# Kernel optimization log

Measured on AMD Instinct MI355X. Metric: run time of the kernel, lower is better.

The kernel has to match this reference:

```python
import jax, jax.numpy as jnp
import numpy as np

B, S, H = 32, 256, 256
D = 2 * H          # BiLSTM output dim (hidden_dim*2)
F = 1024           # total fragment count across the batch
T = 5              # tagset size


def setup_inputs() -> dict:
    key = jax.random.key(0)
    ks = jax.random.split(key, 9)
    en_output = jax.random.normal(ks[0], (B, S, D), jnp.float32)
    # descending lengths, first sentence defines seq_length = S
    lengths = jnp.sort(jax.random.randint(ks[1], (B,), S // 2, S + 1))[::-1]
    lengths = lengths.at[0].set(S)
    frag_b = jax.random.randint(ks[2], (F,), 0, B)
    frag_s = jax.random.randint(ks[3], (F,), 0, S // 2 - 8)
    width = jax.random.randint(ks[4], (F,), 1, 8)
    frag_e = frag_s + width  # end exclusive, always <= lengths[frag_b]
    att_w = jax.random.normal(ks[5], (3 * D, D), jnp.float32) / np.float32(np.sqrt(3 * D))
    att_b = jax.random.normal(ks[6], (3 * D,), jnp.float32) * 0.01
    tag_w = jax.random.normal(ks[7], (T, 4 * D), jnp.float32) / np.float32(np.sqrt(4 * D))
    tag_b = jax.random.normal(ks[8], (T,), jnp.float32) * 0.01
    return {"en_output": en_output, "lengths": lengths, "frag_b": frag_b,
            "frag_s": frag_s, "frag_e": frag_e, "att_w": att_w, "att_b": att_b,
            "tag_w": tag_w, "tag_b": tag_b}


def reference(en_output, lengths, frag_b, frag_s, frag_e, att_w, att_b, tag_w, tag_b):
    Fn = frag_b.shape[0]
    Bn, Sn, Dn = en_output.shape
    dtype = en_output.dtype
    pos = jnp.arange(Sn)                                            # [S]
    in_span = (pos[None, :] >= frag_s[:, None]) & (pos[None, :] < frag_e[:, None])  # [F,S]
    memory = en_output[frag_b]                                      # [F,S,D] gather per fragment
    # word_state = sum of hidden states over the span (segment-sum via mask)
    word_state = jnp.einsum('fs,fsd->fd', in_span.astype(dtype), memory)
    l_word = en_output[frag_b, frag_s]                              # [F,D]
    r_word = en_output[frag_b, frag_e - 1]                          # [F,D]
    span = jnp.concatenate([l_word, word_state, r_word], axis=-1)   # [F,3D]
    # attention mask: the span itself and all padding positions are masked out
    att_mask = in_span | (pos[None, :] >= lengths[frag_b][:, None])  # [F,S]
    seq_len = lengths[0]
    # position distance (int), then position weight 1 - dist/seq_len
    pos_dis = jnp.where(pos[None, :] < frag_s[:, None], frag_s[:, None] - pos[None, :],
                jnp.where(pos[None, :] >= frag_e[:, None], pos[None, :] - frag_e[:, None] + 1,
                          seq_len)).astype(dtype)
    pos_weight = 1.0 - pos_dis / seq_len.astype(dtype)
    final = pos_weight[:, :, None] * memory                         # [F,S,D]
    # att(final) @ span == final @ (att_w.T span) + att_b.span ; att_w is [3D, D] (torch Linear weight)
    v = span @ att_w                                                # [F,D]
    c = span @ att_b                                                # [F]
    scores = jnp.tanh(jnp.einsum('fsd,fd->fs', final, v) + c[:, None])
    scores = jnp.where(att_mask, jnp.asarray(-1e4, dtype), scores)
    att = jax.nn.softmax(scores, axis=1)                            # [F,S]
    mix = jnp.einsum('fs,fsd->fd', att, final)                      # [F,D]
    mix_state = jnp.concatenate([span, mix], axis=-1)               # [F,4D]
    logits = mix_state @ tag_w.T + tag_b                            # [F,T]
    return jax.nn.log_softmax(logits, axis=1)
```

## Files before the change

### kernel.cpp

```cpp
#include <hip/hip_runtime.h>
#include <math.h>

#define BB 32
#define SS 256
#define DD 512
#define FF 1024
#define TT 5
#define K3 1536
#define K4 2048
#define GK 1536
#define SK 4
#define KCH (GK / SK)

__device__ __forceinline__ float wave_reduce_sum(float x) {
#pragma unroll
  for (int o = 32; o > 0; o >>= 1) x += __shfl_xor(x, o);
  return x;
}

__device__ __forceinline__ float fast_tanh(float x) {
  float ax = fabsf(x);
  float t = __expf(-2.f * ax);
  float r = (1.f - t) / (1.f + t);
  return x < 0.f ? -r : r;
}

__global__ __launch_bounds__(1024)
void bucket_kernel(const int* __restrict__ fb, int* __restrict__ order) {
  __shared__ int cnt[BB];
  __shared__ int start[BB];
  int t = threadIdx.x;
  if (t < BB) cnt[t] = 0;
  __syncthreads();
  int b = fb[t];
  int r = atomicAdd(&cnt[b], 1);
  __syncthreads();
  if (t == 0) {
    int acc = 0;
    for (int i = 0; i < BB; ++i) { start[i] = acc; acc += cnt[i]; }
  }
  __syncthreads();
  order[start[b] + r] = t;
}

__global__ __launch_bounds__(128)
void span_kernel(const float* __restrict__ en, const int* __restrict__ fb,
                 const int* __restrict__ fs, const int* __restrict__ fe,
                 const float* __restrict__ att_b,
                 float* __restrict__ span, float* __restrict__ cvec)
{
  int f = blockIdx.x;
  int t = threadIdx.x;
  int b = fb[f], s = fs[f], e = fe[f];
  const float* base = en + (size_t)b * SS * DD;
  int d0 = t * 4;
  float4 lw = *(const float4*)(base + (size_t)s * DD + d0);
  float4 rw = *(const float4*)(base + (size_t)(e - 1) * DD + d0);
  float4 wsum = make_float4(0.f, 0.f, 0.f, 0.f);
  for (int p = s; p < e; ++p) {
    float4 m = *(const float4*)(base + (size_t)p * DD + d0);
    wsum.x += m.x; wsum.y += m.y; wsum.z += m.z; wsum.w += m.w;
  }
  float* sp = span + (size_t)f * K3;
  *(float4*)(sp + d0) = lw;
  *(float4*)(sp + DD + d0) = wsum;
  *(float4*)(sp + 2 * DD + d0) = rw;
  float4 a0 = *(const float4*)(att_b + d0);
  float4 a1 = *(const float4*)(att_b + DD + d0);
  float4 a2 = *(const float4*)(att_b + 2 * DD + d0);
  float part = lw.x*a0.x + lw.y*a0.y + lw.z*a0.z + lw.w*a0.w
             + wsum.x*a1.x + wsum.y*a1.y + wsum.z*a1.z + wsum.w*a1.w
             + rw.x*a2.x + rw.y*a2.y + rw.z*a2.z + rw.w*a2.w;
  part = wave_reduce_sum(part);
  __shared__ float red[2];
  if ((t & 63) == 0) red[t >> 6] = part;
  __syncthreads();
  if (t == 0) cvec[f] = red[0] + red[1];
}

__global__ __launch_bounds__(256)
void gemm_v(const float* __restrict__ A,
            const float* __restrict__ Bw,
            float* __restrict__ Cpart)
{
  const int BM = 32, BN = 64, BK = 16;
  __shared__ float As[BK][BM + 2];
  __shared__ float Bs[BK][BN + 4];
  int t = threadIdx.x;
  int n0 = blockIdx.x * BN;
  int m0 = blockIdx.y * BM;
  int sk = blockIdx.z;
  int kbase = sk * KCH;

  int ar = t >> 3;
  int ac = (t & 7) * 2;
  int br = t >> 4;
  int bc = (t & 15) * 4;
  int tm = (t >> 4) * 2;
  int tn = (t & 15) * 4;

  float acc[2][4] = {};

  for (int k0 = kbase; k0 < kbase + KCH; k0 += BK) {
    float2 av = *(const float2*)(A + (size_t)(m0 + ar) * GK + k0 + ac);
    float4 bv = *(const float4*)(Bw + (size_t)(k0 + br) * DD + n0 + bc);
    __syncthreads();
    As[ac][ar] = av.x;
    As[ac + 1][ar] = av.y;
    *(float4*)(&Bs[br][bc]) = bv;
    __syncthreads();
#pragma unroll
    for (int k = 0; k < BK; ++k) {
      float a0 = As[k][tm], a1 = As[k][tm + 1];
      float4 b = *(float4*)(&Bs[k][tn]);
      acc[0][0] += a0 * b.x; acc[0][1] += a0 * b.y; acc[0][2] += a0 * b.z; acc[0][3] += a0 * b.w;
      acc[1][0] += a1 * b.x; acc[1][1] += a1 * b.y; acc[1][2] += a1 * b.z; acc[1][3] += a1 * b.w;
    }
  }
  float* Cp = Cpart + (size_t)sk * FF * DD;
#pragma unroll
  for (int i = 0; i < 2; ++i) {
    *(float4*)(Cp + (size_t)(m0 + tm + i) * DD + n0 + tn) =
        make_float4(acc[i][0], acc[i][1], acc[i][2], acc[i][3]);
  }
}

__global__ __launch_bounds__(256)
void frag_kernel(const float* __restrict__ en, const int* __restrict__ lengths,
                 const int* __restrict__ fb, const int* __restrict__ fs,
                 const int* __restrict__ fe,
                 const float* __restrict__ span, const float* __restrict__ cvec,
                 const float* __restrict__ vpart,
                 const float* __restrict__ tag_w, const float* __restrict__ tag_b,
                 const int* __restrict__ order,
                 float* __restrict__ out)
{
  __shared__ float v_lds[DD];
  __shared__ float buf[4][DD];
  __shared__ float mstate[4][2];
  __shared__ float mix_lds[DD];
  __shared__ float pl[4 * TT];
  __shared__ float l5[TT];

  int bid = blockIdx.x;
  int f = order[(bid & 7) * (FF / 8) + (bid >> 3)];
  int t = threadIdx.x;
  int lane = t & 63, wv = t >> 6;
  int b = fb[f], s = fs[f], e = fe[f];
  int lenb = lengths[b];
  float seqlen = (float)lengths[0];
  float c = cvec[f];
  const float* mem = en + (size_t)b * SS * DD;

  if (t < 128) {
    float4 v0 = *(const float4*)(vpart + (size_t)f * DD + t * 4);
    float4 v1 = *(const float4*)(vpart + (size_t)FF * DD + (size_t)f * DD + t * 4);
    float4 v2 = *(const float4*)(vpart + 2 * (size_t)FF * DD + (size_t)f * DD + t * 4);
    float4 v3 = *(const float4*)(vpart + 3 * (size_t)FF * DD + (size_t)f * DD + t * 4);
    *(float4*)(v_lds + t * 4) = make_float4(v0.x + v1.x + v2.x + v3.x,
                                            v0.y + v1.y + v2.y + v3.y,
                                            v0.z + v1.z + v2.z + v3.z,
                                            v0.w + v1.w + v2.w + v3.w);
  }
  __syncthreads();

  float4 va = *(float4*)(v_lds + lane * 8);
  float4 vb = *(float4*)(v_lds + lane * 8 + 4);
  float m = -1e30f, ssum = 0.f;
  float am[8] = {0.f, 0.f, 0.f, 0.f, 0.f, 0.f, 0.f, 0.f};

  for (int i0 = 0; i0 < 64; i0 += 8) {
    float4 R0[8], R1[8];
    float d8[8];
#pragma unroll
    for (int k = 0; k < 8; ++k) {
      int p = wv * 64 + i0 + k;
      const float* row = mem + (size_t)p * DD + lane * 8;
      R0[k] = *(const float4*)(row);
      R1[k] = *(const float4*)(row + 4);
      d8[k] = R0[k].x*va.x + R0[k].y*va.y + R0[k].z*va.z + R0[k].w*va.w
            + R1[k].x*vb.x + R1[k].y*vb.y + R1[k].z*vb.z + R1[k].w*vb.w;
    }
#pragma unroll
    for (int o = 32; o > 0; o >>= 1) {
#pragma unroll
      for (int k = 0; k < 8; ++k) d8[k] += __shfl_xor(d8[k], o);
    }
#pragma unroll
    for (int k = 0; k < 8; ++k) {
      int p = wv * 64 + i0 + k;
      bool mask = (p >= s && p < e) || (p >= lenb);
      if (!mask) {
        float dis = (p < s) ? (float)(s - p) : (float)(p - e + 1);
        float pw = 1.f - dis / seqlen;
        float sc = fast_tanh(pw * d8[k] + c);
        if (sc > m) {
          float scale = __expf(m - sc);
          ssum *= scale;
#pragma unroll
          for (int j = 0; j < 8; ++j) am[j] *= scale;
          m = sc;
        }
        float u = __expf(sc - m);
        ssum += u;
        float upw = u * pw;
        am[0] += upw * R0[k].x; am[1] += upw * R0[k].y; am[2] += upw * R0[k].z; am[3] += upw * R0[k].w;
        am[4] += upw * R1[k].x; am[5] += upw * R1[k].y; am[6] += upw * R1[k].z; am[7] += upw * R1[k].w;
      }
    }
  }
  if (lane == 0) { mstate[wv][0] = m; mstate[wv][1] = ssum; }
  __syncthreads();
  float M = fmaxf(fmaxf(mstate[0][0], mstate[1][0]), fmaxf(mstate[2][0], mstate[3][0]));
  float S = mstate[0][1] * __expf(mstate[0][0] - M)
          + mstate[1][1] * __expf(mstate[1][0] - M)
          + mstate[2][1] * __expf(mstate[2][0] - M)
          + mstate[3][1] * __expf(mstate[3][0] - M);
  float ew = __expf(m - M);
  {
    float4 s0 = make_float4(am[0] * ew, am[1] * ew, am[2] * ew, am[3] * ew);
    float4 s1 = make_float4(am[4] * ew, am[5] * ew, am[6] * ew, am[7] * ew);
    *(float4*)(&buf[wv][lane * 8]) = s0;
    *(float4*)(&buf[wv][lane * 8 + 4]) = s1;
  }
  __syncthreads();
  {
    int d0 = t * 2;
    float inv = 1.f / S;
    mix_lds[d0]     = (buf[0][d0] + buf[1][d0] + buf[2][d0] + buf[3][d0]) * inv;
    mix_lds[d0 + 1] = (buf[0][d0 + 1] + buf[1][d0 + 1] + buf[2][d0 + 1] + buf[3][d0 + 1]) * inv;
  }
  __syncthreads();

  float vals[8];
  int idx = t * 8;
  if (idx < K3) {
    const float* sp = span + (size_t)f * K3 + idx;
    float4 x0 = *(const float4*)(sp);
    float4 x1 = *(const float4*)(sp + 4);
    vals[0]=x0.x; vals[1]=x0.y; vals[2]=x0.z; vals[3]=x0.w;
    vals[4]=x1.x; vals[5]=x1.y; vals[6]=x1.z; vals[7]=x1.w;
  } else {
#pragma unroll
    for (int j = 0; j < 8; ++j) vals[j] = mix_lds[idx - K3 + j];
  }
  float acc5[TT];
#pragma unroll
  for (int tg = 0; tg < TT; ++tg) {
    const float* twr = tag_w + (size_t)tg * K4 + idx;
    float a = 0.f;
#pragma unroll
    for (int j = 0; j < 8; ++j) a += vals[j] * twr[j];
    acc5[tg] = wave_reduce_sum(a);
  }
  if (lane == 0) {
#pragma unroll
    for (int tg = 0; tg < TT; ++tg) pl[wv * TT + tg] = acc5[tg];
  }
  __syncthreads();
  if (t < TT) {
    l5[t] = pl[t] + pl[TT + t] + pl[2 * TT + t] + pl[3 * TT + t] + tag_b[t];
  }
  __syncthreads();
  if (t == 0) {
    float mm = l5[0];
#pragma unroll
    for (int j = 1; j < TT; ++j) mm = fmaxf(mm, l5[j]);
    float se = 0.f;
#pragma unroll
    for (int j = 0; j < TT; ++j) se += __expf(l5[j] - mm);
    float lse = mm + logf(se);
#pragma unroll
    for (int j = 0; j < TT; ++j) out[(size_t)f * TT + j] = l5[j] - lse;
  }
}

extern "C" void kernel_launch(void* const* d_in, const int* in_sizes, int n_in,
                              void* d_out, int out_size, void* d_ws, size_t ws_size,
                              hipStream_t stream) {
  const float* en      = (const float*)d_in[0];
  const int*   lengths = (const int*)d_in[1];
  const int*   frag_b  = (const int*)d_in[2];
  const int*   frag_s  = (const int*)d_in[3];
  const int*   frag_e  = (const int*)d_in[4];
  const float* att_w   = (const float*)d_in[5];
  const float* att_b   = (const float*)d_in[6];
  const float* tag_w   = (const float*)d_in[7];
  const float* tag_b   = (const float*)d_in[8];
  float* out = (float*)d_out;

  float* span  = (float*)d_ws;
  float* cvec  = span + (size_t)FF * K3;
  float* vpart = cvec + FF;
  int*   order = (int*)(vpart + (size_t)SK * FF * DD);

  bucket_kernel<<<1, FF, 0, stream>>>(frag_b, order);
  span_kernel<<<FF, 128, 0, stream>>>(en, frag_b, frag_s, frag_e, att_b, span, cvec);
  gemm_v<<<dim3(8, 32, SK), 256, 0, stream>>>(span, att_w, vpart);
  frag_kernel<<<FF, 256, 0, stream>>>(en, lengths, frag_b, frag_s, frag_e,
                                      span, cvec, vpart, tag_w, tag_b, order, out);
}
```

Before: 159.4 us.

## Skip padded rows in attention, enlarge GEMM tile, reorder span blocks

The attention loop now stops at each sentence's valid length instead of loading all 256 rows, so padded positions are never read. The v-GEMM tile grows from 32x64 to 64x64 with a 4x4 register micro-tile, which halves the grid and raises arithmetic per shared-memory load. span_kernel takes its fragment through the batch-bucketed order with an XCD-style interleave, so that fragments sharing a sentence run on nearby blocks and reuse L2. The trade-off is more register pressure in the GEMM and fewer blocks in flight for it.

```diff
diff --git a/kernel.cpp b/kernel.cpp
--- a/kernel.cpp
+++ b/kernel.cpp
@@ -46,10 +46,11 @@
 __global__ __launch_bounds__(128)
 void span_kernel(const float* __restrict__ en, const int* __restrict__ fb,
                  const int* __restrict__ fs, const int* __restrict__ fe,
-                 const float* __restrict__ att_b,
+                 const float* __restrict__ att_b, const int* __restrict__ order,
                  float* __restrict__ span, float* __restrict__ cvec)
 {
-  int f = blockIdx.x;
+  int bid = blockIdx.x;
+  int f = order[(bid & 7) * (FF / 8) + (bid >> 3)];
   int t = threadIdx.x;
   int b = fb[f], s = fs[f], e = fe[f];
   const float* base = en + (size_t)b * SS * DD;
@@ -83,43 +84,46 @@
             const float* __restrict__ Bw,
             float* __restrict__ Cpart)
 {
-  const int BM = 32, BN = 64, BK = 16;
-  __shared__ float As[BK][BM + 2];
+  const int BM = 64, BN = 64, BK = 16;
+  __shared__ float As[BK][BM + 4];
   __shared__ float Bs[BK][BN + 4];
   int t = threadIdx.x;
   int n0 = blockIdx.x * BN;
   int m0 = blockIdx.y * BM;
-  int sk = blockIdx.z;
-  int kbase = sk * KCH;
-
-  int ar = t >> 3;
-  int ac = (t & 7) * 2;
+  int kbase = blockIdx.z * KCH;
+
+  int ar = t >> 2;
+  int ac = (t & 3) * 4;
   int br = t >> 4;
   int bc = (t & 15) * 4;
-  int tm = (t >> 4) * 2;
+  int tm = (t >> 4) * 4;
   int tn = (t & 15) * 4;
 
-  float acc[2][4] = {};
+  float acc[4][4] = {};
 
   for (int k0 = kbase; k0 < kbase + KCH; k0 += BK) {
-    float2 av = *(const float2*)(A + (size_t)(m0 + ar) * GK + k0 + ac);
+    float4 av = *(const float4*)(A  + (size_t)(m0 + ar) * GK + k0 + ac);
     float4 bv = *(const float4*)(Bw + (size_t)(k0 + br) * DD + n0 + bc);
     __syncthreads();
-    As[ac][ar] = av.x;
+    As[ac + 0][ar] = av.x;
     As[ac + 1][ar] = av.y;
+    As[ac + 2][ar] = av.z;
+    As[ac + 3][ar] = av.w;
     *(float4*)(&Bs[br][bc]) = bv;
     __syncthreads();
 #pragma unroll
     for (int k = 0; k < BK; ++k) {
-      float a0 = As[k][tm], a1 = As[k][tm + 1];
+      float4 a = *(float4*)(&As[k][tm]);
       float4 b = *(float4*)(&Bs[k][tn]);
-      acc[0][0] += a0 * b.x; acc[0][1] += a0 * b.y; acc[0][2] += a0 * b.z; acc[0][3] += a0 * b.w;
-      acc[1][0] += a1 * b.x; acc[1][1] += a1 * b.y; acc[1][2] += a1 * b.z; acc[1][3] += a1 * b.w;
+      acc[0][0] += a.x * b.x; acc[0][1] += a.x * b.y; acc[0][2] += a.x * b.z; acc[0][3] += a.x * b.w;
+      acc[1][0] += a.y * b.x; acc[1][1] += a.y * b.y; acc[1][2] += a.y * b.z; acc[1][3] += a.y * b.w;
+      acc[2][0] += a.z * b.x; acc[2][1] += a.z * b.y; acc[2][2] += a.z * b.z; acc[2][3] += a.z * b.w;
+      acc[3][0] += a.w * b.x; acc[3][1] += a.w * b.y; acc[3][2] += a.w * b.z; acc[3][3] += a.w * b.w;
     }
   }
-  float* Cp = Cpart + (size_t)sk * FF * DD;
-#pragma unroll
-  for (int i = 0; i < 2; ++i) {
+  float* Cp = Cpart + (size_t)blockIdx.z * FF * DD;
+#pragma unroll
+  for (int i = 0; i < 4; ++i) {
     *(float4*)(Cp + (size_t)(m0 + tm + i) * DD + n0 + tn) =
         make_float4(acc[i][0], acc[i][1], acc[i][2], acc[i][3]);
   }
@@ -169,17 +173,23 @@
   float m = -1e30f, ssum = 0.f;
   float am[8] = {0.f, 0.f, 0.f, 0.f, 0.f, 0.f, 0.f, 0.f};
 
-  for (int i0 = 0; i0 < 64; i0 += 8) {
+  int rows = lenb - wv * 64;
+  if (rows > 64) rows = 64;
+  for (int i0 = 0; i0 < rows; i0 += 8) {
     float4 R0[8], R1[8];
     float d8[8];
 #pragma unroll
     for (int k = 0; k < 8; ++k) {
-      int p = wv * 64 + i0 + k;
-      const float* row = mem + (size_t)p * DD + lane * 8;
-      R0[k] = *(const float4*)(row);
-      R1[k] = *(const float4*)(row + 4);
-      d8[k] = R0[k].x*va.x + R0[k].y*va.y + R0[k].z*va.z + R0[k].w*va.w
-            + R1[k].x*vb.x + R1[k].y*vb.y + R1[k].z*vb.z + R1[k].w*vb.w;
+      if (i0 + k < rows) {
+        int p = wv * 64 + i0 + k;
+        const float* row = mem + (size_t)p * DD + lane * 8;
+        R0[k] = *(const float4*)(row);
+        R1[k] = *(const float4*)(row + 4);
+        d8[k] = R0[k].x*va.x + R0[k].y*va.y + R0[k].z*va.z + R0[k].w*va.w
+              + R1[k].x*vb.x + R1[k].y*vb.y + R1[k].z*vb.z + R1[k].w*vb.w;
+      } else {
+        d8[k] = 0.f;
+      }
     }
 #pragma unroll
     for (int o = 32; o > 0; o >>= 1) {
@@ -189,8 +199,8 @@
 #pragma unroll
     for (int k = 0; k < 8; ++k) {
       int p = wv * 64 + i0 + k;
-      bool mask = (p >= s && p < e) || (p >= lenb);
-      if (!mask) {
+      bool live = (i0 + k < rows) && !(p >= s && p < e);
+      if (live) {
         float dis = (p < s) ? (float)(s - p) : (float)(p - e + 1);
         float pw = 1.f - dis / seqlen;
         float sc = fast_tanh(pw * d8[k] + c);
@@ -295,8 +305,8 @@
   int*   order = (int*)(vpart + (size_t)SK * FF * DD);
 
   bucket_kernel<<<1, FF, 0, stream>>>(frag_b, order);
-  span_kernel<<<FF, 128, 0, stream>>>(en, frag_b, frag_s, frag_e, att_b, span, cvec);
-  gemm_v<<<dim3(8, 32, SK), 256, 0, stream>>>(span, att_w, vpart);
+  span_kernel<<<FF, 128, 0, stream>>>(en, frag_b, frag_s, frag_e, att_b, order, span, cvec);
+  gemm_v<<<dim3(8, 16, SK), 256, 0, stream>>>(span, att_w, vpart);
   frag_kernel<<<FF, 256, 0, stream>>>(en, lengths, frag_b, frag_s, frag_e,
                                       span, cvec, vpart, tag_w, tag_b, order, out);
 }
```

Result: no change. 156.2 us (-2.0%).
